# Optimization experiments

Hardware: AMD Instinct MI355X
Metric: run time of the kernel (lower is better)

Reference implementation:

```python
import jax, jax.numpy as jnp
import numpy as np


def _hard_sigmoid(x):
    # Keras ConvLSTM2D default recurrent_activation
    return jnp.clip(0.2 * x + 0.5, 0.0, 1.0)


def _conv_same(x, w):
    # x: [B,H,W,Cin], w: [kh,kw,Cin,Cout]
    return jax.lax.conv_general_dilated(
        x, w, window_strides=(1, 1), padding='SAME',
        dimension_numbers=('NHWC', 'HWIO', 'NHWC'))


def setup_inputs() -> dict:
    key = jax.random.key(0)
    ks = jax.random.split(key, 6)
    B, T, H, W, F = 16, 16, 64, 64, 64
    return {
        'inputs': jax.random.normal(ks[0], (B, T, H, W, 1), jnp.float32),  # only T is used
        'h0': jax.random.normal(ks[1], (B, H, W, F), jnp.float32),
        'c0': jax.random.normal(ks[2], (B, H, W, F), jnp.float32),
        'kernels': jax.random.normal(ks[3], (T, 3, 3, F, 4 * F), jnp.float32) * 0.05,
        'rec_kernels': jax.random.normal(ks[4], (T, 3, 3, F, 4 * F), jnp.float32) * 0.05,
        'bias': jnp.zeros((T, 4 * F), jnp.float32),
    }


def reference(inputs, h0, c0, kernels, rec_kernels, bias):
    # The layer feeds h back as the cell input each step, so the cell input x == h.
    # By linearity, conv(h, Wk) + conv(h, Uk) == conv(h, Wk + Uk); we fuse the two convs.
    # Gate order (Keras ConvLSTM2DCell): i, f, c, o.
    def step(carry, params):
        h, c = carry
        Wk, Uk, b = params  # [3,3,F,4F], [3,3,F,4F], [4F]
        z = _conv_same(h, Wk + Uk) + b  # [B,H,W,4F]
        zi, zf, zc, zo = jnp.split(z, 4, axis=-1)
        i = _hard_sigmoid(zi)
        f = _hard_sigmoid(zf)
        c_new = f * c + i * jnp.tanh(zc)
        o = _hard_sigmoid(zo)
        h_new = o * jnp.tanh(c_new)
        return (h_new, c_new), h_new

    (_, _), hs = jax.lax.scan(step, (h0, c0), (kernels, rec_kernels, bias))
    return jnp.moveaxis(hs, 0, 1)  # [B, T, H, W, F]
```

## Files before the change

kernel.cpp:

```cpp
#include <hip/hip_runtime.h>
#include <math.h>

typedef _Float16 f16;
typedef _Float16 f16x4 __attribute__((ext_vector_type(4)));
typedef _Float16 f16x8 __attribute__((ext_vector_type(8)));
typedef float f32x4 __attribute__((ext_vector_type(4)));

#define NB 16
#define NT 16
#define NH 64
#define NW 64
#define NF 64
#define NG 256
#define HWF ((size_t)NH * NW * NF)
#define OUT_BSTRIDE ((size_t)NT * HWF)
#define RS2 8448
#define ZS 258
#define WSTEP ((size_t)18432)

#define MFMA(a, b, c) __builtin_amdgcn_mfma_f32_16x16x32_f16((a), (b), (c), 0, 0, 0)

__device__ __forceinline__ void gload_lds16(const void* g, void* l) {
    __builtin_amdgcn_global_load_lds(
        (const __attribute__((address_space(1))) unsigned int*)(g),
        (__attribute__((address_space(3))) unsigned int*)(l), 16, 0, 0);
}

__device__ __forceinline__ float hsig(float x) {
    return fminf(fmaxf(0.2f * x + 0.5f, 0.0f), 1.0f);
}

__device__ __forceinline__ float ftanh(float x) {
    float t = __builtin_amdgcn_exp2f(x * 2.885390081777927f);
    return 1.0f - 2.0f * __builtin_amdgcn_rcpf(t + 1.0f);
}

__global__ void fuse_w_hi(const float* __restrict__ k, const float* __restrict__ rk,
                          f16* __restrict__ wf2) {
    int idx = blockIdx.x * 256 + threadIdx.x;
    if (idx >= NT * 9 * NG * 8) return;
    int g8   = idx & 7;
    int cout = (idx >> 3) & 255;
    int tt   = idx >> 11;
    int tap  = tt % 9;
    int t    = tt / 9;
    int kk = g8 >> 2, lg = g8 & 3;

    const float* ks = k  + (size_t)tt * NF * NG + cout;
    const float* rs = rk + (size_t)tt * NF * NG + cout;

    f16 hi8[8];
#pragma unroll
    for (int j = 0; j < 8; ++j) {
        int cin = kk * 32 + lg * 8 + j;
        hi8[j] = (f16)(ks[(size_t)cin * NG] + rs[(size_t)cin * NG]);
    }
    const int lane = lg * 16 + (cout & 15);
    size_t chunk = (size_t)t * WSTEP + (size_t)(tap * 2 + kk) * 1024 +
                   (size_t)(cout >> 4) * 64 + lane;
    *(f16x8*)&wf2[chunk * 8] = *(f16x8*)hi8;
}

__global__ void f32_to_f16(const float* __restrict__ src, f16* __restrict__ dst, int n4) {
    int i = blockIdx.x * 256 + threadIdx.x;
    if (i >= n4) return;
    float4 v = ((const float4*)src)[i];
    f16x4 o = { (f16)v.x, (f16)v.y, (f16)v.z, (f16)v.w };
    *(f16x4*)&dst[(size_t)i * 4] = o;
}

__global__ void __launch_bounds__(512, 4)
convlstm_mfma_step(const f16* __restrict__ h2in, f16* __restrict__ h2out,
                   f16* __restrict__ cbuf,
                   float* __restrict__ hout,
                   const f16* __restrict__ wt,
                   const float* __restrict__ bias)
{
    __shared__ __align__(16) unsigned char lds[67584];

    const int tid  = threadIdx.x;
    const int w    = tid >> 6;
    const int lane = tid & 63;
    const int bb   = blockIdx.y;
    const int y0   = blockIdx.x * 2;

    if (tid < 64) {
        int row = tid >> 4, side = (tid >> 3) & 1, j = tid & 7;
        *(f16x8*)&lds[row * RS2 + side * (65 * 128) + j * 16] = (f16x8)(_Float16)0.0f;
    }

    {
        const int r    = w >> 1;
        const int gy   = y0 - 1 + r;
        const int half = w & 1;
        const unsigned dbase = r * RS2 + 128 + half * 4096;
        if (gy >= 0 && gy < NH) {
            const unsigned char* gsrc = (const unsigned char*)h2in +
                ((((size_t)bb * NH + gy) * NW) << 7);
#pragma unroll
            for (int i = 0; i < 4; ++i) {
                const int xrel = half * 32 + i * 8 + (lane >> 3);
                const unsigned src = ((unsigned)xrel << 7) +
                    ((unsigned)((lane & 7) ^ ((xrel + 1) & 7)) << 4);
                gload_lds16(gsrc + src, (void*)&lds[dbase + i * 1024]);
            }
        } else {
            const f16x8 zf = (f16x8)(_Float16)0.0f;
#pragma unroll
            for (int i = 0; i < 4; ++i)
                *(f16x8*)&lds[dbase + i * 1024 + lane * 16] = zf;
        }
    }
    __syncthreads();

    const int wm = w >> 2;
    const int wn = w & 3;
    const int lm = lane & 15;
    const int lg = lane >> 4;

    f32x4 acc[4][4];
#pragma unroll
    for (int mf = 0; mf < 4; ++mf)
#pragma unroll
        for (int nf = 0; nf < 4; ++nf) acc[mf][nf] = (f32x4)0.0f;

    unsigned av[3][2];
#pragma unroll
    for (int d = 0; d < 3; ++d)
#pragma unroll
        for (int kk = 0; kk < 2; ++kk) {
            const int tx = lm + d;
            av[d][kk] = (unsigned)(tx * 128 +
                        (((kk * 4 + lg) ^ (tx & 7)) << 4));
        }

    const f16x8* wb = (const f16x8*)wt + (size_t)(wn * 4) * 64 + lane;

    f16x8 bh[4];
#pragma unroll
    for (int it = 0; it < 18; ++it) {
        const int tap = it >> 1, kk = it & 1;
#pragma unroll
        for (int nf = 0; nf < 4; ++nf)
            bh[nf] = wb[(size_t)it * 1024 + nf * 64];
        const int ty = tap / 3;
        const int d  = tap - ty * 3;
        const unsigned abase = (unsigned)((wm + ty) * RS2) + av[d][kk];
        __builtin_amdgcn_s_setprio(1);
#pragma unroll
        for (int mf = 0; mf < 4; ++mf) {
            const f16x8 ah = *(const f16x8*)&lds[abase + mf * 2048];
#pragma unroll
            for (int nf = 0; nf < 4; ++nf)
                acc[mf][nf] = MFMA(ah, bh[nf], acc[mf][nf]);
        }
        __builtin_amdgcn_s_setprio(0);
    }

    __syncthreads();

    float* zbuf = (float*)lds;
    const int f = tid & 63;
    const float bi = bias[f], bfv = bias[64 + f], bcv = bias[128 + f], bov = bias[192 + f];

#pragma unroll 1
    for (int half = 0; half < 2; ++half) {
        if (wm == half) {
#pragma unroll
            for (int mf = 0; mf < 4; ++mf)
#pragma unroll
                for (int nf = 0; nf < 4; ++nf)
#pragma unroll
                    for (int j = 0; j < 4; ++j)
                        zbuf[(mf * 16 + lg * 4 + j) * ZS + wn * 64 + nf * 16 + lm] =
                            acc[mf][nf][j];
        }
        __syncthreads();
        const int gy = y0 + half;
#pragma unroll 1
        for (int k2 = 0; k2 < 8; ++k2) {
            const int x = (tid >> 6) + k2 * 8;
            const float* zz = zbuf + x * ZS;
            float zi  = zz[f]       + bi;
            float zfv = zz[64 + f]  + bfv;
            float zc  = zz[128 + f] + bcv;
            float zo  = zz[192 + f] + bov;
            size_t goff = (((size_t)bb * NH + gy) * NW + x) * NF + f;
            float cp = (float)cbuf[goff];
            float ig = hsig(zi), fg = hsig(zfv), og = hsig(zo);
            float cn = fg * cp + ig * ftanh(zc);
            cbuf[goff] = (f16)cn;
            float hn = og * ftanh(cn);
            hout[(size_t)bb * OUT_BSTRIDE + (((size_t)gy * NW + x) * NF + f)] = hn;
            h2out[goff] = (f16)hn;
        }
        __syncthreads();
    }
}

extern "C" void kernel_launch(void* const* d_in, const int* in_sizes, int n_in,
                              void* d_out, int out_size, void* d_ws, size_t ws_size,
                              hipStream_t stream) {
    const float* h0    = (const float*)d_in[1];
    const float* c0    = (const float*)d_in[2];
    const float* kern  = (const float*)d_in[3];
    const float* rkern = (const float*)d_in[4];
    const float* bias  = (const float*)d_in[5];
    float* out = (float*)d_out;

    f16* wf2   = (f16*)d_ws;
    f16* h2a   = wf2 + (size_t)NT * WSTEP * 8;
    f16* h2b   = h2a + (size_t)NB * HWF;
    f16* cbuf  = h2b + (size_t)NB * HWF;

    const int n4 = (int)(NB * HWF / 4);
    fuse_w_hi<<<(NT * 9 * NG * 8 + 255) / 256, 256, 0, stream>>>(kern, rkern, wf2);
    f32_to_f16<<<(n4 + 255) / 256, 256, 0, stream>>>(h0, h2a, n4);
    f32_to_f16<<<(n4 + 255) / 256, 256, 0, stream>>>(c0, cbuf, n4);

    dim3 grid(NH / 2, NB);
    for (int t = 0; t < NT; ++t) {
        const f16* hin = (t & 1) ? h2b : h2a;
        f16* hnx       = (t & 1) ? h2a : h2b;
        convlstm_mfma_step<<<grid, 512, 0, stream>>>(
            hin, hnx, cbuf,
            out + (size_t)t * HWF,
            wf2 + (size_t)t * WSTEP * 8,
            bias + t * NG);
    }
}
```

Measured before the change: 468.2 us.

## Shrink conv-step blocks to one output row with 256 threads and remapped grid

Each block now computes a single output row with 4 waves instead of two rows with 8 waves, halving LDS to about 33 KB and doubling the grid to 1024 blocks. The 1D block index is remapped so that consecutive blocks span different batch images in an XCD-aware interleave. The epilogue writes gate values in two 32-column halves to fit the smaller LDS. This aims for more resident blocks and better spread across compute units, but each output row now loads three input rows, so halo reloads of h rise from 4 rows per 2 outputs to 3 rows per output.

```diff
diff --git a/kernel.cpp b/kernel.cpp
--- a/kernel.cpp
+++ b/kernel.cpp
@@ -69,37 +69,37 @@
     *(f16x4*)&dst[(size_t)i * 4] = o;
 }
 
-__global__ void __launch_bounds__(512, 4)
+__global__ void __launch_bounds__(256, 4)
 convlstm_mfma_step(const f16* __restrict__ h2in, f16* __restrict__ h2out,
                    f16* __restrict__ cbuf,
                    float* __restrict__ hout,
                    const f16* __restrict__ wt,
                    const float* __restrict__ bias)
 {
-    __shared__ __align__(16) unsigned char lds[67584];
+    __shared__ __align__(16) unsigned char lds[33024];
 
     const int tid  = threadIdx.x;
     const int w    = tid >> 6;
     const int lane = tid & 63;
-    const int bb   = blockIdx.y;
-    const int y0   = blockIdx.x * 2;
-
-    if (tid < 64) {
+
+    const int id = blockIdx.x;
+    const int bb = ((id & 7) << 1) + ((id >> 9) & 1);
+    const int y0 = (id >> 3) & 63;
+
+    if (tid < 48) {
         int row = tid >> 4, side = (tid >> 3) & 1, j = tid & 7;
         *(f16x8*)&lds[row * RS2 + side * (65 * 128) + j * 16] = (f16x8)(_Float16)0.0f;
     }
 
-    {
-        const int r    = w >> 1;
-        const int gy   = y0 - 1 + r;
-        const int half = w & 1;
-        const unsigned dbase = r * RS2 + 128 + half * 4096;
+    if (w < 3) {
+        const int gy = y0 - 1 + w;
+        const unsigned dbase = w * RS2 + 128;
         if (gy >= 0 && gy < NH) {
             const unsigned char* gsrc = (const unsigned char*)h2in +
                 ((((size_t)bb * NH + gy) * NW) << 7);
 #pragma unroll
-            for (int i = 0; i < 4; ++i) {
-                const int xrel = half * 32 + i * 8 + (lane >> 3);
+            for (int i = 0; i < 8; ++i) {
+                const int xrel = i * 8 + (lane >> 3);
                 const unsigned src = ((unsigned)xrel << 7) +
                     ((unsigned)((lane & 7) ^ ((xrel + 1) & 7)) << 4);
                 gload_lds16(gsrc + src, (void*)&lds[dbase + i * 1024]);
@@ -107,14 +107,12 @@
         } else {
             const f16x8 zf = (f16x8)(_Float16)0.0f;
 #pragma unroll
-            for (int i = 0; i < 4; ++i)
+            for (int i = 0; i < 8; ++i)
                 *(f16x8*)&lds[dbase + i * 1024 + lane * 16] = zf;
         }
     }
     __syncthreads();
 
-    const int wm = w >> 2;
-    const int wn = w & 3;
     const int lm = lane & 15;
     const int lg = lane >> 4;
 
@@ -134,7 +132,7 @@
                         (((kk * 4 + lg) ^ (tx & 7)) << 4));
         }
 
-    const f16x8* wb = (const f16x8*)wt + (size_t)(wn * 4) * 64 + lane;
+    const f16x8* wb = (const f16x8*)wt + (size_t)(w * 4) * 64 + lane;
 
     f16x8 bh[4];
 #pragma unroll
@@ -145,7 +143,7 @@
             bh[nf] = wb[(size_t)it * 1024 + nf * 64];
         const int ty = tap / 3;
         const int d  = tap - ty * 3;
-        const unsigned abase = (unsigned)((wm + ty) * RS2) + av[d][kk];
+        const unsigned abase = (unsigned)(ty * RS2) + av[d][kk];
         __builtin_amdgcn_s_setprio(1);
 #pragma unroll
         for (int mf = 0; mf < 4; ++mf) {
@@ -164,34 +162,34 @@
     const float bi = bias[f], bfv = bias[64 + f], bcv = bias[128 + f], bov = bias[192 + f];
 
 #pragma unroll 1
-    for (int half = 0; half < 2; ++half) {
-        if (wm == half) {
-#pragma unroll
-            for (int mf = 0; mf < 4; ++mf)
-#pragma unroll
-                for (int nf = 0; nf < 4; ++nf)
-#pragma unroll
-                    for (int j = 0; j < 4; ++j)
-                        zbuf[(mf * 16 + lg * 4 + j) * ZS + wn * 64 + nf * 16 + lm] =
-                            acc[mf][nf][j];
+    for (int xp = 0; xp < 2; ++xp) {
+#pragma unroll
+        for (int m2 = 0; m2 < 2; ++m2) {
+            const int mf = xp * 2 + m2;
+#pragma unroll
+            for (int nf = 0; nf < 4; ++nf)
+#pragma unroll
+                for (int j = 0; j < 4; ++j)
+                    zbuf[(m2 * 16 + lg * 4 + j) * ZS + w * 64 + nf * 16 + lm] =
+                        acc[mf][nf][j];
         }
         __syncthreads();
-        const int gy = y0 + half;
 #pragma unroll 1
         for (int k2 = 0; k2 < 8; ++k2) {
-            const int x = (tid >> 6) + k2 * 8;
-            const float* zz = zbuf + x * ZS;
+            const int xl = (tid >> 6) + k2 * 4;
+            const int x  = xp * 32 + xl;
+            const float* zz = zbuf + xl * ZS;
             float zi  = zz[f]       + bi;
             float zfv = zz[64 + f]  + bfv;
             float zc  = zz[128 + f] + bcv;
             float zo  = zz[192 + f] + bov;
-            size_t goff = (((size_t)bb * NH + gy) * NW + x) * NF + f;
+            size_t goff = (((size_t)bb * NH + y0) * NW + x) * NF + f;
             float cp = (float)cbuf[goff];
             float ig = hsig(zi), fg = hsig(zfv), og = hsig(zo);
             float cn = fg * cp + ig * ftanh(zc);
             cbuf[goff] = (f16)cn;
             float hn = og * ftanh(cn);
-            hout[(size_t)bb * OUT_BSTRIDE + (((size_t)gy * NW + x) * NF + f)] = hn;
+            hout[(size_t)bb * OUT_BSTRIDE + (((size_t)y0 * NW + x) * NF + f)] = hn;
             h2out[goff] = (f16)hn;
         }
         __syncthreads();
@@ -218,11 +216,10 @@
     f32_to_f16<<<(n4 + 255) / 256, 256, 0, stream>>>(h0, h2a, n4);
     f32_to_f16<<<(n4 + 255) / 256, 256, 0, stream>>>(c0, cbuf, n4);
 
-    dim3 grid(NH / 2, NB);
     for (int t = 0; t < NT; ++t) {
         const f16* hin = (t & 1) ? h2b : h2a;
         f16* hnx       = (t & 1) ? h2a : h2b;
-        convlstm_mfma_step<<<grid, 512, 0, stream>>>(
+        convlstm_mfma_step<<<dim3(NH * NB), 256, 0, stream>>>(
             hin, hnx, cbuf,
             out + (size_t)t * HWF,
             wf2 + (size_t)t * WSTEP * 8,
```

After: 739.9 us. 1.58x slower.
